# Kernel tuning notes

Measured on AMD Instinct MI355X. Metric: run time of the kernel, lower is better.

The kernel has to match this reference:

```python
import jax, jax.numpy as jnp
import numpy as np

IMAGE_SIZE = 128
RADIUS = 0.02
POINTS_PER_PIXEL = 16
FOV_DEG = 60.0
ZNEAR = 1.0
DIST = 2.0
R2 = RADIUS * RADIUS


def setup_inputs() -> dict:
    key = jax.random.key(0)
    k1, k2, k3 = jax.random.split(key, 3)
    B, N = 2, 2048
    points = jax.random.normal(k1, (B, N, 3), jnp.float32) * 0.35  # cloud fits in frustum
    eye = jax.random.normal(k2, (B, 3), jnp.float32)
    eye = eye / jnp.linalg.norm(eye, axis=-1, keepdims=True) * DIST  # camera at distance DIST
    colors = jax.random.uniform(k3, (B, N, 3), jnp.float32)
    return {"points": points, "eye": eye, "colors": colors}


def _look_at_rotation(eye):
    # PyTorch3D look_at: at=origin, up=+y; R columns are camera x/y/z axes.
    up = jnp.broadcast_to(jnp.array([0.0, 1.0, 0.0], jnp.float32), eye.shape)
    z = -eye
    z = z / jnp.linalg.norm(z, axis=-1, keepdims=True)
    x = jnp.cross(up, z)
    x = x / jnp.linalg.norm(x, axis=-1, keepdims=True)
    y = jnp.cross(z, x)
    return jnp.stack([x, y, z], axis=-1)  # [B,3,3]


def _render(points, eye, colors):
    B, N, _ = points.shape
    S = IMAGE_SIZE
    K = POINTS_PER_PIXEL
    R = _look_at_rotation(eye)
    cam = jnp.einsum('bnd,bde->bne', points - eye[:, None, :], R)  # world -> view
    focal = 1.0 / jnp.tan(jnp.deg2rad(FOV_DEG) / 2.0)  # FoV perspective, fov=60deg
    z = cam[..., 2]
    zs = jnp.where(z > 0, z, 1.0)  # behind-camera points are culled below
    x_ndc = cam[..., 0] * focal / zs
    y_ndc = cam[..., 1] * focal / zs
    visible = z > ZNEAR
    # pixel centers in PyTorch3D NDC (+x left, +y up)
    grid = 1.0 - (2.0 * jnp.arange(S, dtype=jnp.float32) + 1.0) / S
    px = jnp.tile(grid[None, :], (S, 1)).reshape(-1)  # [P], P = S*S
    py = jnp.tile(grid[:, None], (1, S)).reshape(-1)
    # squared NDC distance pixel-center -> projected point: [B, P, N]
    d2 = (px[None, :, None] - x_ndc[:, None, :]) ** 2 + (py[None, :, None] - y_ndc[:, None, :]) ** 2
    hit = (d2 < R2) & visible[:, None, :]
    score = jnp.where(hit, z[:, None, :], jnp.inf)
    neg_z, idx = jax.lax.top_k(-score, K)  # K nearest-in-depth hits per pixel (z-buffer)
    valid = jnp.isfinite(neg_z)  # [B,P,K]
    d2k = jnp.take_along_axis(d2, idx, axis=-1)
    alpha = jnp.where(valid, jnp.clip(1.0 - d2k / R2, 0.0, 1.0), 0.0)
    feat = jax.vmap(lambda c, i: c[i])(colors, idx)  # [B,P,K,3]
    # front-to-back alpha compositing (AlphaCompositor)
    trans = jnp.cumprod(1.0 - alpha, axis=-1)
    trans = jnp.concatenate([jnp.ones_like(trans[..., :1]), trans[..., :-1]], axis=-1)
    w = alpha * trans
    img = jnp.einsum('bpk,bpkc->bpc', w, feat)
    return img.reshape(B, S, S, 3)


def reference(points, eye, colors):
    return _render(points, eye, colors)
```

## Files before the change

kernel.cpp:

```cpp
#include <hip/hip_runtime.h>
#include <hip/hip_bf16.h>

#define S_IMG    128
#define KTOP     16
#define RAD2     (0.02f*0.02f)
#define INV_R2   (1.0f/RAD2)
#define RADF     0.02f
#define ZNEARF   1.0f
#define FOCALF   1.7320508075688772f
#define TPI      16
#define NTILE    (TPI*TPI)
#define TPB      256
#define CAP      256
#define KSENT    0xFFFFFFFFu

__global__ __launch_bounds__(TPB) void render_tile8(
    const float* __restrict__ points,
    const float* __restrict__ eye,
    const float* __restrict__ colors,
    float* __restrict__ out,
    int N)
{
    __shared__ float s_cx[CAP];
    __shared__ float s_cy[CAP];
    __shared__ __align__(16) unsigned s_key[CAP + 8];
    __shared__ __align__(16) float2   s_sxy [CAP + 16];
    __shared__ __align__(16) float4   s_scol[CAP + 16];
    __shared__ int s_cnt;

    const int tid = threadIdx.x;
    const int blk = blockIdx.x;
    const int b   = blk >> 8;
    const int t   = blk & 255;
    const int ty  = t >> 4, tx = t & 15;

    const float ex = eye[b*3+0], ey = eye[b*3+1], ez = eye[b*3+2];
    const float zinv = 1.0f / sqrtf(ex*ex + ey*ey + ez*ez);
    const float zax = -ex*zinv, zay = -ey*zinv, zaz = -ez*zinv;
    const float xinv = 1.0f / sqrtf(zaz*zaz + zax*zax);
    const float xax = zaz*xinv, xaz = -zax*xinv;
    const float yax = zay*xaz;
    const float yay = zaz*xax - zax*xaz;
    const float yaz = -zay*xax;

    const float cx = 1.0f - (float)(2*(tx*8) + 8) / S_IMG;
    const float cy = 1.0f - (float)(2*(ty*8) + 8) / S_IMG;
    const float hx = 7.0f / S_IMG + RADF + 1e-6f;
    const float hy = 7.0f / S_IMG + RADF + 1e-6f;

    if (tid == 0) s_cnt = 0;
    __syncthreads();

    const float* pts = points + b*N*3;
    #pragma unroll 4
    for (int j = tid; j < N; j += TPB) {
        float wx = pts[3*j+0] - ex;
        float wy = pts[3*j+1] - ey;
        float wz = pts[3*j+2] - ez;
        float cz = wx*zax + wy*zay + wz*zaz;
        if (cz > ZNEARF) {
            float inv = FOCALF / cz;
            float xn = (wx*xax + wz*xaz) * inv;
            float yn = (wx*yax + wy*yay + wz*yaz) * inv;
            if (fabsf(xn - cx) <= hx && fabsf(yn - cy) <= hy) {
                int slot = atomicAdd(&s_cnt, 1);
                if (slot < CAP) {
                    s_cx [slot] = xn;
                    s_cy [slot] = yn;
                    s_key[slot] = (__float_as_uint(cz) & ~2047u) | (unsigned)j;
                }
            }
        }
    }
    __syncthreads();
    int M = s_cnt; if (M > CAP) M = CAP;

    if (tid < 16) {
        if (tid < 8) s_key[M + tid] = KSENT;
        s_sxy [M + tid] = make_float2(1.0e9f, 1.0e9f);
        s_scol[M + tid] = make_float4(0.f, 0.f, 0.f, 0.f);
    }
    __syncthreads();

    const float* cols = colors + b*N*3;
    if (tid < M) {
        const unsigned mk = s_key[tid];
        const float ux = s_cx[tid], uy = s_cy[tid];
        const uint4* k4 = reinterpret_cast<const uint4*>(s_key);
        const int nb = (M + 7) >> 3;
        int rank = 0;
        for (int q = 0; q < nb; ++q) {
            uint4 a  = k4[2*q];
            uint4 bb = k4[2*q+1];
            rank += (int)(a.x <mk) + (int)(a.y <mk) + (int)(a.z <mk) + (int)(a.w <mk)
                  + (int)(bb.x<mk) + (int)(bb.y<mk) + (int)(bb.z<mk) + (int)(bb.w<mk);
        }
        const int pi = (int)(mk & 2047u);
        s_sxy [rank] = make_float2(ux, uy);
        s_scol[rank] = make_float4(cols[3*pi+0], cols[3*pi+1], cols[3*pi+2], 0.0f);
    }
    __syncthreads();

    const int sub = tid & 3;
    const int p   = tid >> 2;
    const int row = ty*8 + (p >> 3);
    const int col = tx*8 + (p & 7);
    const float pxc = 1.0f - (2.0f*col + 1.0f) / S_IMG;
    const float pyc = 1.0f - (2.0f*row + 1.0f) / S_IMG;

    const int L = 4 * ((M + 15) >> 4);
    const int base = sub * L;

    const float4* xy4 = reinterpret_cast<const float4*>(s_sxy);
    float T = 1.0f, r = 0.0f, g = 0.0f, bl = 0.0f;
    int hits = 0;
    for (int i = 0; i < L; i += 4) {
        const int ii = base + i;
        float4 u   = xy4[(ii >> 1) + 0];
        float4 v   = xy4[(ii >> 1) + 1];
        float4 c0v = s_scol[ii + 0];
        float4 c1v = s_scol[ii + 1];
        float4 c2v = s_scol[ii + 2];
        float4 c3v = s_scol[ii + 3];
        float dx, dy, d2, a, w; bool h;

        dx = pxc - u.x; dy = pyc - u.y; d2 = dx*dx + dy*dy;
        h = (d2 < RAD2); hits += h ? 1 : 0;
        a = h ? 1.0f - d2 * INV_R2 : 0.0f;
        w = a * T; r += w*c0v.x; g += w*c0v.y; bl += w*c0v.z; T -= T*a;

        dx = pxc - u.z; dy = pyc - u.w; d2 = dx*dx + dy*dy;
        h = (d2 < RAD2); hits += h ? 1 : 0;
        a = h ? 1.0f - d2 * INV_R2 : 0.0f;
        w = a * T; r += w*c1v.x; g += w*c1v.y; bl += w*c1v.z; T -= T*a;

        dx = pxc - v.x; dy = pyc - v.y; d2 = dx*dx + dy*dy;
        h = (d2 < RAD2); hits += h ? 1 : 0;
        a = h ? 1.0f - d2 * INV_R2 : 0.0f;
        w = a * T; r += w*c2v.x; g += w*c2v.y; bl += w*c2v.z; T -= T*a;

        dx = pxc - v.z; dy = pyc - v.w; d2 = dx*dx + dy*dy;
        h = (d2 < RAD2); hits += h ? 1 : 0;
        a = h ? 1.0f - d2 * INV_R2 : 0.0f;
        w = a * T; r += w*c3v.x; g += w*c3v.y; bl += w*c3v.z; T -= T*a;
    }

    #pragma unroll
    for (int mk2 = 1; mk2 <= 2; mk2 <<= 1) {
        float pr = __shfl_xor(r,  mk2, 64);
        float pg = __shfl_xor(g,  mk2, 64);
        float pb = __shfl_xor(bl, mk2, 64);
        float pT = __shfl_xor(T,  mk2, 64);
        int   ph = __shfl_xor(hits, mk2, 64);
        const bool lower = (sub & mk2) == 0;
        r  = lower ? r  + T*pr : pr + pT*r;
        g  = lower ? g  + T*pg : pg + pT*g;
        bl = lower ? bl + T*pb : pb + pT*bl;
        T  = lower ? T*pT      : pT*T;
        hits += ph;
    }

    if (sub == 0) {
        if (hits > KTOP) {
            T = 1.0f; r = 0.0f; g = 0.0f; bl = 0.0f;
            int hh = 0;
            for (int i = 0; i < M && hh < KTOP; ++i) {
                float2 xy = s_sxy[i];
                float dx = pxc - xy.x, dy = pyc - xy.y;
                float d2 = dx*dx + dy*dy;
                if (d2 < RAD2) {
                    float4 cc = s_scol[i];
                    float a = 1.0f - d2 * INV_R2;
                    float w = a * T;
                    r += w*cc.x; g += w*cc.y; bl += w*cc.z;
                    T -= T*a; ++hh;
                }
            }
        }
        const int gpix = b * (S_IMG*S_IMG) + row * S_IMG + col;
        float* o = out + (size_t)gpix * 3;
        o[0] = r; o[1] = g; o[2] = bl;
    }
}

extern "C" void kernel_launch(void* const* d_in, const int* in_sizes, int n_in,
                              void* d_out, int out_size, void* d_ws, size_t ws_size,
                              hipStream_t stream)
{
    const float* points = (const float*)d_in[0];
    const float* eye    = (const float*)d_in[1];
    const float* colors = (const float*)d_in[2];
    float* out = (float*)d_out;

    const int B = in_sizes[1] / 3;
    const int N = in_sizes[0] / (3 * B);

    render_tile8<<<B * NTILE, TPB, 0, stream>>>(points, eye, colors, out, N);
}
```

Before: 15.03 us.

## Double block size, split compositing across 8 subs, aggregate culling atomics per wave

```diff
diff --git a/kernel.cpp b/kernel.cpp
--- a/kernel.cpp
+++ b/kernel.cpp
@@ -10,7 +10,8 @@
 #define FOCALF   1.7320508075688772f
 #define TPI      16
 #define NTILE    (TPI*TPI)
-#define TPB      256
+#define TPB      512
+#define SUBS     8
 #define CAP      256
 #define KSENT    0xFFFFFFFFu
 
@@ -24,15 +25,16 @@
     __shared__ float s_cx[CAP];
     __shared__ float s_cy[CAP];
     __shared__ __align__(16) unsigned s_key[CAP + 8];
-    __shared__ __align__(16) float2   s_sxy [CAP + 16];
-    __shared__ __align__(16) float4   s_scol[CAP + 16];
+    __shared__ __align__(16) float2   s_sxy [CAP + 32];
+    __shared__ __align__(16) float4   s_scol[CAP + 32];
     __shared__ int s_cnt;
 
-    const int tid = threadIdx.x;
-    const int blk = blockIdx.x;
-    const int b   = blk >> 8;
-    const int t   = blk & 255;
-    const int ty  = t >> 4, tx = t & 15;
+    const int tid  = threadIdx.x;
+    const int lane = tid & 63;
+    const int blk  = blockIdx.x;
+    const int b    = blk >> 8;
+    const int t    = blk & 255;
+    const int ty   = t >> 4, tx = t & 15;
 
     const float ex = eye[b*3+0], ey = eye[b*3+1], ez = eye[b*3+2];
     const float zinv = 1.0f / sqrtf(ex*ex + ey*ey + ez*ez);
@@ -51,23 +53,41 @@
     if (tid == 0) s_cnt = 0;
     __syncthreads();
 
-    const float* pts = points + b*N*3;
-    #pragma unroll 4
-    for (int j = tid; j < N; j += TPB) {
-        float wx = pts[3*j+0] - ex;
-        float wy = pts[3*j+1] - ey;
-        float wz = pts[3*j+2] - ez;
-        float cz = wx*zax + wy*zay + wz*zaz;
-        if (cz > ZNEARF) {
-            float inv = FOCALF / cz;
-            float xn = (wx*xax + wz*xaz) * inv;
-            float yn = (wx*yax + wy*yay + wz*yaz) * inv;
-            if (fabsf(xn - cx) <= hx && fabsf(yn - cy) <= hy) {
-                int slot = atomicAdd(&s_cnt, 1);
-                if (slot < CAP) {
-                    s_cx [slot] = xn;
-                    s_cy [slot] = yn;
-                    s_key[slot] = (__float_as_uint(cz) & ~2047u) | (unsigned)j;
+    const float4* pq = reinterpret_cast<const float4*>(points + b*N*3);
+    const int nquad = N >> 2;
+    for (int qd = tid; qd < nquad; qd += TPB) {
+        float4 A  = pq[3*qd+0];
+        float4 Bv = pq[3*qd+1];
+        float4 C  = pq[3*qd+2];
+        float qx[4] = {A.x, A.w, Bv.z, C.y};
+        float qy[4] = {A.y, Bv.x, Bv.w, C.z};
+        float qz[4] = {A.z, Bv.y, C.x, C.w};
+        #pragma unroll
+        for (int u = 0; u < 4; ++u) {
+            float wx = qx[u] - ex, wy = qy[u] - ey, wz = qz[u] - ez;
+            float cz = wx*zax + wy*zay + wz*zaz;
+            float xn = 0.f, yn = 0.f;
+            bool keep = (cz > ZNEARF);
+            if (keep) {
+                float inv = FOCALF / cz;
+                xn = (wx*xax + wz*xaz) * inv;
+                yn = (wx*yax + wy*yay + wz*yaz) * inv;
+                keep = (fabsf(xn - cx) <= hx) && (fabsf(yn - cy) <= hy);
+            }
+            unsigned long long act = __ballot(keep);
+            if (act) {
+                int lead = (int)__ffsll(act) - 1;
+                int base = 0;
+                if (lane == lead) base = atomicAdd(&s_cnt, __popcll(act));
+                base = __shfl(base, lead, 64);
+                if (keep) {
+                    int slot = base + __popcll(act & ((1ull << lane) - 1ull));
+                    if (slot < CAP) {
+                        s_cx [slot] = xn;
+                        s_cy [slot] = yn;
+                        s_key[slot] = (__float_as_uint(cz) & ~2047u)
+                                    | (unsigned)(4*qd + u);
+                    }
                 }
             }
         }
@@ -75,7 +95,7 @@
     __syncthreads();
     int M = s_cnt; if (M > CAP) M = CAP;
 
-    if (tid < 16) {
+    if (tid < 32) {
         if (tid < 8) s_key[M + tid] = KSENT;
         s_sxy [M + tid] = make_float2(1.0e9f, 1.0e9f);
         s_scol[M + tid] = make_float4(0.f, 0.f, 0.f, 0.f);
@@ -101,14 +121,14 @@
     }
     __syncthreads();
 
-    const int sub = tid & 3;
-    const int p   = tid >> 2;
+    const int sub = tid & (SUBS-1);
+    const int p   = tid >> 3;
     const int row = ty*8 + (p >> 3);
     const int col = tx*8 + (p & 7);
     const float pxc = 1.0f - (2.0f*col + 1.0f) / S_IMG;
     const float pyc = 1.0f - (2.0f*row + 1.0f) / S_IMG;
 
-    const int L = 4 * ((M + 15) >> 4);
+    const int L    = 4 * ((M + 31) >> 5);
     const int base = sub * L;
 
     const float4* xy4 = reinterpret_cast<const float4*>(s_sxy);
@@ -146,13 +166,13 @@
     }
 
     #pragma unroll
-    for (int mk2 = 1; mk2 <= 2; mk2 <<= 1) {
-        float pr = __shfl_xor(r,  mk2, 64);
-        float pg = __shfl_xor(g,  mk2, 64);
-        float pb = __shfl_xor(bl, mk2, 64);
-        float pT = __shfl_xor(T,  mk2, 64);
-        int   ph = __shfl_xor(hits, mk2, 64);
-        const bool lower = (sub & mk2) == 0;
+    for (int mx = 1; mx <= 4; mx <<= 1) {
+        float pr = __shfl_xor(r,  mx, 64);
+        float pg = __shfl_xor(g,  mx, 64);
+        float pb = __shfl_xor(bl, mx, 64);
+        float pT = __shfl_xor(T,  mx, 64);
+        int   ph = __shfl_xor(hits, mx, 64);
+        const bool lower = (sub & mx) == 0;
         r  = lower ? r  + T*pr : pr + pT*r;
         g  = lower ? g  + T*pg : pg + pT*g;
         bl = lower ? bl + T*pb : pb + pT*bl;
```

Measured after the change: 14.28 us. -5.0%, faster.
